# Performance work log

Measured on AMD Instinct MI355X. Metric: run time of the kernel, lower is better.

The kernel has to match this reference:

```python
import jax, jax.numpy as jnp
import numpy as np

B, LP, LQ, H = 32, 2048, 512, 1024

def setup_inputs() -> dict:
    key = jax.random.key(0)
    k1, k2, k3, k4 = jax.random.split(key, 4)
    p_encode = jax.random.normal(k1, (B, LP, H), dtype=jnp.float32)
    q_encode = jax.random.normal(k2, (B, LQ, H), dtype=jnp.float32)
    # nn.Linear(H, H): weight [out, in], bias [out]
    bound = 1.0 / np.sqrt(H)
    G_weight = jax.random.uniform(k3, (H, H), dtype=jnp.float32, minval=-bound, maxval=bound)
    G_bias = jax.random.uniform(k4, (H,), dtype=jnp.float32, minval=-bound, maxval=bound)
    return {"p_encode": p_encode, "q_encode": q_encode, "G_weight": G_weight, "G_bias": G_bias}

def reference(p_encode, q_encode, G_weight, G_bias):
    # q_project = transpose(G(q_encode), -2, -1): [B, H, LQ]
    q_proj = jnp.einsum('bqh,oh->bqo', q_encode, G_weight) + G_bias  # [B, LQ, H]
    # att_matrix = bmm(p_encode, q_project^T): [B, LP, LQ]
    att = jnp.einsum('bph,bqh->bpq', p_encode, q_proj)
    # m_p = softmax over LQ (dim=-1) @ q_encode -> [B, LP, H]
    m_p = jnp.einsum('bpq,bqh->bph', jax.nn.softmax(att, axis=-1), q_encode)
    # m_q = softmax over LP (dim=-2), transposed, @ p_encode -> [B, LQ, H]
    m_q = jnp.einsum('bpq,bph->bqh', jax.nn.softmax(att, axis=-2), p_encode)
    return (m_p, m_q)
```

## Files before the change

kernel.cpp:

```cpp
#include <hip/hip_runtime.h>

typedef _Float16 half_t;
typedef _Float16 f16x8 __attribute__((ext_vector_type(8)));
typedef _Float16 f16x4 __attribute__((ext_vector_type(4)));
typedef float    f32x4 __attribute__((ext_vector_type(4)));
typedef float    f32x16 __attribute__((ext_vector_type(16)));

typedef const __attribute__((address_space(1))) void cg_void;
typedef __attribute__((address_space(3))) void lds_void;

#define BB 32
#define LP 2048
#define LQ 512
#define HH 1024

enum { M_QPROJ = 0, M_OUT32 = 1 };

__global__ void cvt16_k(const float* __restrict__ w, half_t* __restrict__ o) {
  long i = ((long)blockIdx.x * 256 + threadIdx.x) * 4;
  f32x4 v = *(const f32x4*)(w + i);
  f16x4 h;
  h[0] = (half_t)v[0]; h[1] = (half_t)v[1]; h[2] = (half_t)v[2]; h[3] = (half_t)v[3];
  *(f16x4*)(o + i) = h;
}

__global__ __launch_bounds__(256) void dualcvt_k(const float* __restrict__ in,
                                                 half_t* __restrict__ rm,
                                                 half_t* __restrict__ tr,
                                                 int R, int C) {
  __shared__ half_t tile[64 * 64];
  const long zb = blockIdx.z;
  const float* src = in + zb * (long)R * C;
  half_t* dstT = tr + zb * (long)C * R;
  half_t* dstR = rm + zb * (long)R * C;
  const int r0 = blockIdx.y * 64, c0 = blockIdx.x * 64;
  const int t = threadIdx.x;
  const int cl = (t & 15) * 4;
  const int rl = t >> 4;
#pragma unroll
  for (int rr = 0; rr < 4; rr++) {
    int r = rr * 16 + rl;
    f32x4 v = *(const f32x4*)(src + (long)(r0 + r) * C + c0 + cl);
    f16x4 h;
#pragma unroll
    for (int j = 0; j < 4; j++) {
      h[j] = (half_t)v[j];
      int c = cl + j;
      tile[c * 64 + (r ^ (((c >> 3) & 7) << 3))] = h[j];
    }
    *(f16x4*)(dstR + (long)(r0 + r) * C + c0 + cl) = h;
  }
  __syncthreads();
  const int c = t >> 2;
  const int rch = (t & 3) * 16;
  const int m = (c >> 3) & 7;
  const int B0 = c * 64 + (rch ^ ((m << 3) & 48));
  const int hi = (m & 1) << 3;
  f16x8 g0 = *(const f16x8*)&tile[B0 + hi];
  f16x8 g1 = *(const f16x8*)&tile[B0 + (8 ^ hi)];
  half_t* dp = dstT + (long)(c0 + c) * R + r0 + rch;
  *(f16x8*)dp = g0;
  *(f16x8*)(dp + 8) = g1;
}

__global__ __launch_bounds__(256) void cfin_k(const float* __restrict__ pmg,
                                              const float* __restrict__ psg,
                                              float* __restrict__ cmax,
                                              float* __restrict__ cinv) {
  long i = (long)blockIdx.x * 256 + threadIdx.x;
  long b = i / LQ, q = i - b * LQ;
  const float* mp = pmg + (b * 16) * LQ + q;
  const float* sp = psg + (b * 16) * LQ + q;
  float m = -3e38f, s = 0.f;
#pragma unroll
  for (int t = 0; t < 16; t++) {
    float mm = mp[(long)t * LQ], ss = sp[(long)t * LQ];
    float nm = fmaxf(m, mm);
    s = s * __expf(m - nm) + ss * __expf(mm - nm);
    m = nm;
  }
  cmax[i] = m;
  cinv[i] = 1.f / s;
}

__global__ __launch_bounds__(256) void pq_k(const half_t* __restrict__ E,
                                            half_t* __restrict__ out,
                                            const float* __restrict__ pmg,
                                            const float* __restrict__ cmax,
                                            const float* __restrict__ cinv) {
  __shared__ half_t tile[64 * 64];
  const long zb = blockIdx.z;
  const half_t* src = E + zb * (long)LP * LQ;
  half_t* dst = out + zb * (long)LQ * LP;
  const int r0 = blockIdx.y * 64, c0 = blockIdx.x * 64;
  const int tIdx = r0 >> 7;
  const int t = threadIdx.x;
  const int cl = (t & 15) * 4;
  const int rl = t >> 4;
  f32x4 tm = *(const f32x4*)(pmg + ((long)zb * 16 + tIdx) * LQ + c0 + cl);
  f32x4 cm = *(const f32x4*)(cmax + (long)zb * LQ + c0 + cl);
  f32x4 ci = *(const f32x4*)(cinv + (long)zb * LQ + c0 + cl);
  float sc[4];
#pragma unroll
  for (int j = 0; j < 4; j++) sc[j] = __expf(tm[j] - cm[j]) * ci[j];
#pragma unroll
  for (int rr = 0; rr < 4; rr++) {
    int r = rr * 16 + rl;
    f16x4 v = *(const f16x4*)(src + (long)(r0 + r) * LQ + c0 + cl);
#pragma unroll
    for (int j = 0; j < 4; j++) {
      float x = (float)v[j] * sc[j];
      int c = cl + j;
      tile[c * 64 + (r ^ (((c >> 3) & 7) << 3))] = (half_t)x;
    }
  }
  __syncthreads();
  const int c = t >> 2;
  const int rch = (t & 3) * 16;
  const int m = (c >> 3) & 7;
  const int B0 = c * 64 + (rch ^ ((m << 3) & 48));
  const int hi = (m & 1) << 3;
  f16x8 g0 = *(const f16x8*)&tile[B0 + hi];
  f16x8 g1 = *(const f16x8*)&tile[B0 + (8 ^ hi)];
  half_t* dp = dst + (long)(c0 + c) * LP + r0 + rch;
  *(f16x8*)dp = g0;
  *(f16x8*)(dp + 8) = g1;
}

template<int ROWS>
__device__ __forceinline__ void stage_op(const half_t* src, int ld,
                                         half_t* lds_base, int wid, int lane) {
  const int goff = (((lane & 3) ^ ((lane >> 3) & 3)) << 3);
#pragma unroll
  for (int j = 0; j < ROWS / 128; ++j) {
    int row = j * 128 + wid * 16 + (lane >> 2);
    const half_t* g = src + (long)row * ld + goff;
    __builtin_amdgcn_global_load_lds((cg_void*)g,
        (lds_void*)(lds_base + j * 4096 + wid * 512), 16, 0, 0);
  }
}

__device__ __forceinline__ void xcd_swz(long lid, long nwg, long& out) {
  const long q8 = nwg >> 3, r8 = nwg & 7;
  const long xcd = lid & 7, rest = lid >> 3;
  out = (xcd < r8 ? xcd * (q8 + 1) : r8 * (q8 + 1) + (xcd - r8) * q8) + rest;
}

__global__ __launch_bounds__(512, 2) void attf_k(
    const half_t* __restrict__ Ap,
    const half_t* __restrict__ Bp,
    half_t* __restrict__ PpO,
    half_t* __restrict__ EO,
    float* __restrict__ pmg, float* __restrict__ psg) {
  __shared__ __align__(16) half_t As[3 * 4096];
  __shared__ __align__(16) half_t Bs[3 * 16384];
  __shared__ float rmL[4][128];
  __shared__ float cmL[2][512];
  __shared__ float rsL[4][128];
  __shared__ float csL[2][512];

  const int nby = gridDim.y;
  long lid;
  xcd_swz(blockIdx.y + (long)nby * blockIdx.z, (long)nby * gridDim.z, lid);
  const int by = (int)(lid % nby);
  const int bz = (int)(lid / nby);

  const int t0 = threadIdx.x;
  const int lane = t0 & 63;
  const int wid = t0 >> 6;
  const int wm = wid >> 2, wn = wid & 3;
  const int m0 = by * 128;

  const half_t* Abase = Ap + ((long)bz * LP + m0) * HH;
  const half_t* Bbase = Bp + (long)bz * LQ * HH;

  const int c5 = lane & 31, hi = lane >> 5;
  const int sx = (c5 >> 1) & 3;
  const int ofs0 = c5 * 32 + ((hi ^ sx) << 3);
  const int ofs1 = c5 * 32 + (((2 | hi) ^ sx) << 3);

  f32x16 acc[2][4] = {};
  const int NT = HH / 32;

#pragma unroll
  for (int tt = 0; tt < 2; ++tt) {
    stage_op<128>(Abase + tt * 32, HH, As + tt * 4096, wid, lane);
    stage_op<512>(Bbase + tt * 32, HH, Bs + tt * 16384, wid, lane);
  }

  for (int t = 0; t < NT; ++t) {
    if (t + 1 < NT) asm volatile("s_waitcnt vmcnt(5)" ::: "memory");
    else            asm volatile("s_waitcnt vmcnt(0)" ::: "memory");
    __builtin_amdgcn_s_barrier();
    asm volatile("" ::: "memory");

    const half_t* Au = As + (t % 3) * 4096;
    const half_t* Bu = Bs + (t % 3) * 16384;
    f16x8 af[2][2], bf[4][2];
#pragma unroll
    for (int mf = 0; mf < 2; ++mf) {
      const half_t* p = Au + (wm * 64 + mf * 32) * 32;
      af[mf][0] = *(const f16x8*)(p + ofs0);
      af[mf][1] = *(const f16x8*)(p + ofs1);
    }
#pragma unroll
    for (int nf = 0; nf < 4; ++nf) {
      const half_t* p = Bu + (wn * 128 + nf * 32) * 32;
      bf[nf][0] = *(const f16x8*)(p + ofs0);
      bf[nf][1] = *(const f16x8*)(p + ofs1);
    }
    if (t + 2 < NT) {
      const int u2 = (t + 2) % 3;
      stage_op<128>(Abase + (t + 2) * 32, HH, As + u2 * 4096, wid, lane);
      stage_op<512>(Bbase + (t + 2) * 32, HH, Bs + u2 * 16384, wid, lane);
    }
    __builtin_amdgcn_s_setprio(1);
#pragma unroll
    for (int mf = 0; mf < 2; ++mf)
#pragma unroll
      for (int nf = 0; nf < 4; ++nf) {
        acc[mf][nf] = __builtin_amdgcn_mfma_f32_32x32x16_f16(af[mf][0], bf[nf][0], acc[mf][nf], 0, 0, 0);
        acc[mf][nf] = __builtin_amdgcn_mfma_f32_32x32x16_f16(af[mf][1], bf[nf][1], acc[mf][nf], 0, 0, 0);
      }
    __builtin_amdgcn_s_setprio(0);
  }

  float rmv[2][16], cmv[4];
#pragma unroll
  for (int m = 0; m < 2; ++m)
#pragma unroll
    for (int r = 0; r < 16; ++r) {
      float v = fmaxf(fmaxf(acc[m][0][r], acc[m][1][r]), fmaxf(acc[m][2][r], acc[m][3][r]));
#pragma unroll
      for (int o = 1; o < 32; o <<= 1) v = fmaxf(v, __shfl_xor(v, o, 64));
      rmv[m][r] = v;
    }
#pragma unroll
  for (int n = 0; n < 4; ++n) {
    float v = acc[0][n][0];
#pragma unroll
    for (int m = 0; m < 2; ++m)
#pragma unroll
      for (int r = 0; r < 16; ++r) v = fmaxf(v, acc[m][n][r]);
    v = fmaxf(v, __shfl_xor(v, 32, 64));
    cmv[n] = v;
  }
  if (c5 < 16) {
#pragma unroll
    for (int m = 0; m < 2; ++m)
      rmL[wn][wm * 64 + m * 32 + (c5 & 3) + 8 * (c5 >> 2) + 4 * hi] = rmv[m][c5];
  }
  if (hi == 0) {
#pragma unroll
    for (int n = 0; n < 4; ++n) cmL[wm][wn * 128 + n * 32 + c5] = cmv[n];
  }
  __syncthreads();
  if (t0 < 128)
    rmL[0][t0] = fmaxf(fmaxf(rmL[0][t0], rmL[1][t0]), fmaxf(rmL[2][t0], rmL[3][t0]));
  {
    float cm2 = fmaxf(cmL[0][t0 & 511], cmL[1][t0 & 511]);
    cmL[0][t0 & 511] = cm2;
    pmg[((long)bz * 16 + by) * LQ + (t0 & 511)] = cm2;
  }
  __syncthreads();
#pragma unroll
  for (int m = 0; m < 2; ++m)
#pragma unroll
    for (int r = 0; r < 16; ++r)
      rmv[m][r] = rmL[0][wm * 64 + m * 32 + (r & 3) + 8 * (r >> 2) + 4 * hi];
#pragma unroll
  for (int n = 0; n < 4; ++n) cmv[n] = cmL[0][wn * 128 + n * 32 + c5];

  half_t* EB = EO + (long)bz * LP * LQ;
  float csW[4] = {0.f, 0.f, 0.f, 0.f};
  float rowS[2][16];
#pragma unroll
  for (int m = 0; m < 2; ++m)
#pragma unroll
    for (int r = 0; r < 16; ++r) {
      long grow = (long)(m0 + wm * 64 + m * 32 + (r & 3) + 8 * (r >> 2) + 4 * hi) * LQ;
      float s = 0.f;
#pragma unroll
      for (int n = 0; n < 4; ++n) {
        float a = acc[m][n][r];
        float e = __expf(a - cmv[n]);
        float p = __expf(a - rmv[m][r]);
        csW[n] += e;
        EB[grow + wn * 128 + n * 32 + c5] = (half_t)e;
        acc[m][n][r] = p;
        s += p;
      }
#pragma unroll
      for (int o = 1; o < 32; o <<= 1) s += __shfl_xor(s, o, 64);
      rowS[m][r] = s;
    }
#pragma unroll
  for (int n = 0; n < 4; ++n) csW[n] += __shfl_xor(csW[n], 32, 64);
  if (c5 < 16) {
#pragma unroll
    for (int m = 0; m < 2; ++m)
      rsL[wn][wm * 64 + m * 32 + (c5 & 3) + 8 * (c5 >> 2) + 4 * hi] = rowS[m][c5];
  }
  if (hi == 0) {
#pragma unroll
    for (int n = 0; n < 4; ++n) csL[wm][wn * 128 + n * 32 + c5] = csW[n];
  }
  __syncthreads();
  if (t0 < 128)
    rsL[0][t0] = 1.f / (rsL[0][t0] + rsL[1][t0] + rsL[2][t0] + rsL[3][t0]);
  psg[((long)bz * 16 + by) * LQ + (t0 & 511)] = csL[0][t0 & 511] + csL[1][t0 & 511];
  __syncthreads();

  half_t* PpB = PpO + (long)bz * LP * LQ;
#pragma unroll
  for (int m = 0; m < 2; ++m)
#pragma unroll
    for (int r = 0; r < 16; ++r) {
      int row = wm * 64 + m * 32 + (r & 3) + 8 * (r >> 2) + 4 * hi;
      long grow = (long)(m0 + row) * LQ;
      float ri = rsL[0][row];
#pragma unroll
      for (int n = 0; n < 4; ++n)
        PpB[grow + wn * 128 + n * 32 + c5] = (half_t)(acc[m][n][r] * ri);
    }
}

template<int MODE, int BM>
__global__ __launch_bounds__(512, 2) void gemm_k(
    const half_t* __restrict__ Ap, const half_t* __restrict__ Bp, void* __restrict__ Cp,
    const float* __restrict__ bias,
    int lda, int ldb, int ldc, int K,
    long sA, long sB, long sC) {
  constexpr int NMF = BM / 64;
  constexpr int AS = BM * 32;
  __shared__ __align__(16) half_t As[4 * AS];
  __shared__ __align__(16) half_t Bs[4 * 8192];

  const int nbx = gridDim.x, nby = gridDim.y;
  long lid;
  xcd_swz(blockIdx.x + (long)nbx * (blockIdx.y + (long)nby * blockIdx.z),
          (long)nbx * nby * gridDim.z, lid);
  const int bx = (int)(lid % nbx);
  const long tmp = lid / nbx;
  const int by = (int)(tmp % nby);
  const int bz = (int)(tmp / nby);

  const int t0 = threadIdx.x;
  const int lane = t0 & 63;
  const int wid = t0 >> 6;
  const int wm = wid >> 2, wn = wid & 3;
  const int m0 = by * BM, n0 = bx * 256;

  const half_t* Abase = Ap + sA * bz + (long)m0 * lda;
  const half_t* Bbase = Bp + sB * bz + (long)n0 * ldb;

  const int c5 = lane & 31, hi = lane >> 5;
  const int sx = (c5 >> 1) & 3;
  const int ofs0 = c5 * 32 + ((hi ^ sx) << 3);
  const int ofs1 = c5 * 32 + (((2 | hi) ^ sx) << 3);

  f32x16 acc[NMF][2] = {};
  const int NT = K >> 5;

#pragma unroll
  for (int tt = 0; tt < 3; ++tt) {
    stage_op<BM>(Abase + tt * 32, lda, As + tt * AS, wid, lane);
    stage_op<256>(Bbase + tt * 32, ldb, Bs + tt * 8192, wid, lane);
  }

  for (int t = 0; t < NT; ++t) {
    if (t + 2 < NT) {
      if constexpr (BM == 256) asm volatile("s_waitcnt vmcnt(8)" ::: "memory");
      else                     asm volatile("s_waitcnt vmcnt(6)" ::: "memory");
    } else if (t + 1 < NT) {
      if constexpr (BM == 256) asm volatile("s_waitcnt vmcnt(4)" ::: "memory");
      else                     asm volatile("s_waitcnt vmcnt(3)" ::: "memory");
    } else {
      asm volatile("s_waitcnt vmcnt(0)" ::: "memory");
    }
    __builtin_amdgcn_s_barrier();
    asm volatile("" ::: "memory");

    const half_t* Au = As + (t & 3) * AS;
    const half_t* Bu = Bs + (t & 3) * 8192;
    f16x8 af[NMF][2], bf[2][2];
#pragma unroll
    for (int mf = 0; mf < NMF; ++mf) {
      const half_t* p = Au + (wm * (BM / 2) + mf * 32) * 32;
      af[mf][0] = *(const f16x8*)(p + ofs0);
      af[mf][1] = *(const f16x8*)(p + ofs1);
    }
#pragma unroll
    for (int nf = 0; nf < 2; ++nf) {
      const half_t* p = Bu + (wn * 64 + nf * 32) * 32;
      bf[nf][0] = *(const f16x8*)(p + ofs0);
      bf[nf][1] = *(const f16x8*)(p + ofs1);
    }
    if (t + 3 < NT) {
      const int u3 = (t + 3) & 3;
      stage_op<BM>(Abase + (t + 3) * 32, lda, As + u3 * AS, wid, lane);
      stage_op<256>(Bbase + (t + 3) * 32, ldb, Bs + u3 * 8192, wid, lane);
    }
    __builtin_amdgcn_s_setprio(1);
#pragma unroll
    for (int mf = 0; mf < NMF; ++mf)
#pragma unroll
      for (int nf = 0; nf < 2; ++nf) {
        acc[mf][nf] = __builtin_amdgcn_mfma_f32_32x32x16_f16(af[mf][0], bf[nf][0], acc[mf][nf], 0, 0, 0);
        acc[mf][nf] = __builtin_amdgcn_mfma_f32_32x32x16_f16(af[mf][1], bf[nf][1], acc[mf][nf], 0, 0, 0);
      }
    __builtin_amdgcn_s_setprio(0);
  }

#pragma unroll
  for (int nf = 0; nf < 2; ++nf) {
    int col = n0 + wn * 64 + nf * 32 + c5;
    float bv = 0.f;
    if constexpr (MODE == M_QPROJ) bv = bias[col];
#pragma unroll
    for (int mf = 0; mf < NMF; ++mf) {
      int rbase = m0 + wm * (BM / 2) + mf * 32 + 4 * hi;
#pragma unroll
      for (int r = 0; r < 16; ++r) {
        int row = rbase + (r & 3) + 8 * (r >> 2);
        if constexpr (MODE == M_QPROJ)
          ((half_t*)Cp)[(long)row * ldc + col] = (half_t)(acc[mf][nf][r] + bv);
        else
          ((float*)Cp)[sC * bz + (long)row * ldc + col] = acc[mf][nf][r];
      }
    }
  }
}

extern "C" void kernel_launch(void* const* d_in, const int* in_sizes, int n_in,
                              void* d_out, int out_size, void* d_ws, size_t ws_size,
                              hipStream_t stream) {
  const float* p_enc = (const float*)d_in[0];
  const float* q_enc = (const float*)d_in[1];
  const float* Gw    = (const float*)d_in[2];
  const float* Gb    = (const float*)d_in[3];
  float* m_p = (float*)d_out;
  float* m_q = m_p + (long)BB * LP * HH;

  half_t* w16   = (half_t*)d_ws;
  half_t* q16   = w16 + (long)HH * HH;
  half_t* qT16  = q16 + (long)BB * LQ * HH;
  half_t* qpj16 = qT16 + (long)BB * HH * LQ;
  half_t* p16   = qpj16 + (long)BB * LQ * HH;
  half_t* pT16  = p16 + (long)BB * LP * HH;
  half_t* Pp    = pT16 + (long)BB * HH * LP;
  half_t* Ebuf  = Pp + (long)BB * LP * LQ;
  half_t* Pq    = Ebuf + (long)BB * LP * LQ;
  float*  cmaxb = (float*)(Pq + (long)BB * LQ * LP);
  float*  cinvb = cmaxb + (long)BB * LQ;
  float*  pmg   = cinvb + (long)BB * LQ;
  float*  psg   = pmg + (long)BB * 16 * LQ;

  cvt16_k<<<HH * HH / 1024, 256, 0, stream>>>(Gw, w16);

  dualcvt_k<<<dim3(HH / 64, LQ / 64, BB), 256, 0, stream>>>(q_enc, q16, qT16, LQ, HH);

  gemm_k<M_QPROJ, 256><<<dim3(HH / 256, BB * LQ / 256, 1), 512, 0, stream>>>(
      q16, w16, qpj16, Gb, HH, HH, HH, HH, 0, 0, 0);

  dualcvt_k<<<dim3(HH / 64, LP / 64, BB), 256, 0, stream>>>(p_enc, p16, pT16, LP, HH);

  attf_k<<<dim3(1, LP / 128, BB), 512, 0, stream>>>(p16, qpj16, Pp, Ebuf, pmg, psg);

  cfin_k<<<BB * LQ / 256, 256, 0, stream>>>(pmg, psg, cmaxb, cinvb);
  pq_k<<<dim3(LQ / 64, LP / 64, BB), 256, 0, stream>>>(Ebuf, Pq, pmg, cmaxb, cinvb);

  gemm_k<M_OUT32, 256><<<dim3(HH / 256, LP / 256, BB), 512, 0, stream>>>(
      Pp, qT16, m_p, nullptr, LQ, LQ, HH, LQ,
      (long)LP * LQ, (long)HH * LQ, (long)LP * HH);

  gemm_k<M_OUT32, 256><<<dim3(HH / 256, LQ / 256, BB), 512, 0, stream>>>(
      Pq, pT16, m_q, nullptr, LP, LP, HH, LP,
      (long)LQ * LP, (long)HH * LP, (long)LQ * HH);
}
```

Before: 535.4 us.

## Merge conversion, column-softmax finalize, and output GEMM launches into fewer kernels

```diff
diff --git a/kernel.cpp b/kernel.cpp
--- a/kernel.cpp
+++ b/kernel.cpp
@@ -24,16 +24,23 @@
   *(f16x4*)(o + i) = h;
 }
 
-__global__ __launch_bounds__(256) void dualcvt_k(const float* __restrict__ in,
-                                                 half_t* __restrict__ rm,
-                                                 half_t* __restrict__ tr,
-                                                 int R, int C) {
+__global__ __launch_bounds__(256) void cvt2_k(const float* __restrict__ qe,
+                                              half_t* __restrict__ q16o,
+                                              half_t* __restrict__ qT16o,
+                                              const float* __restrict__ pe,
+                                              half_t* __restrict__ p16o,
+                                              half_t* __restrict__ pT16o) {
   __shared__ half_t tile[64 * 64];
+  const int byg = blockIdx.y;
+  const float* in; half_t* rm; half_t* tr; int R, r0;
+  if (byg < 8) { in = qe; rm = q16o; tr = qT16o; R = LQ; r0 = byg * 64; }
+  else         { in = pe; rm = p16o; tr = pT16o; R = LP; r0 = (byg - 8) * 64; }
+  const int C = HH;
   const long zb = blockIdx.z;
   const float* src = in + zb * (long)R * C;
   half_t* dstT = tr + zb * (long)C * R;
   half_t* dstR = rm + zb * (long)R * C;
-  const int r0 = blockIdx.y * 64, c0 = blockIdx.x * 64;
+  const int c0 = blockIdx.x * 64;
   const int t = threadIdx.x;
   const int cl = (t & 15) * 4;
   const int rl = t >> 4;
@@ -63,31 +70,10 @@
   *(f16x8*)(dp + 8) = g1;
 }
 
-__global__ __launch_bounds__(256) void cfin_k(const float* __restrict__ pmg,
-                                              const float* __restrict__ psg,
-                                              float* __restrict__ cmax,
-                                              float* __restrict__ cinv) {
-  long i = (long)blockIdx.x * 256 + threadIdx.x;
-  long b = i / LQ, q = i - b * LQ;
-  const float* mp = pmg + (b * 16) * LQ + q;
-  const float* sp = psg + (b * 16) * LQ + q;
-  float m = -3e38f, s = 0.f;
-#pragma unroll
-  for (int t = 0; t < 16; t++) {
-    float mm = mp[(long)t * LQ], ss = sp[(long)t * LQ];
-    float nm = fmaxf(m, mm);
-    s = s * __expf(m - nm) + ss * __expf(mm - nm);
-    m = nm;
-  }
-  cmax[i] = m;
-  cinv[i] = 1.f / s;
-}
-
-__global__ __launch_bounds__(256) void pq_k(const half_t* __restrict__ E,
-                                            half_t* __restrict__ out,
-                                            const float* __restrict__ pmg,
-                                            const float* __restrict__ cmax,
-                                            const float* __restrict__ cinv) {
+__global__ __launch_bounds__(256) void pq2_k(const half_t* __restrict__ E,
+                                             half_t* __restrict__ out,
+                                             const float* __restrict__ pmg,
+                                             const float* __restrict__ psg) {
   __shared__ half_t tile[64 * 64];
   const long zb = blockIdx.z;
   const half_t* src = E + zb * (long)LP * LQ;
@@ -97,12 +83,26 @@
   const int t = threadIdx.x;
   const int cl = (t & 15) * 4;
   const int rl = t >> 4;
-  f32x4 tm = *(const f32x4*)(pmg + ((long)zb * 16 + tIdx) * LQ + c0 + cl);
-  f32x4 cm = *(const f32x4*)(cmax + (long)zb * LQ + c0 + cl);
-  f32x4 ci = *(const f32x4*)(cinv + (long)zb * LQ + c0 + cl);
+
+  float m4[4] = {-3e38f, -3e38f, -3e38f, -3e38f}, s4[4] = {0.f, 0.f, 0.f, 0.f};
+  const float* mpb = pmg + (long)zb * 16 * LQ + c0 + cl;
+  const float* spb = psg + (long)zb * 16 * LQ + c0 + cl;
+#pragma unroll
+  for (int tt = 0; tt < 16; ++tt) {
+    f32x4 mm = *(const f32x4*)(mpb + (long)tt * LQ);
+    f32x4 ss = *(const f32x4*)(spb + (long)tt * LQ);
+#pragma unroll
+    for (int j = 0; j < 4; ++j) {
+      float nm = fmaxf(m4[j], mm[j]);
+      s4[j] = s4[j] * __expf(m4[j] - nm) + ss[j] * __expf(mm[j] - nm);
+      m4[j] = nm;
+    }
+  }
+  f32x4 tm = *(const f32x4*)(mpb + (long)tIdx * LQ);
   float sc[4];
 #pragma unroll
-  for (int j = 0; j < 4; j++) sc[j] = __expf(tm[j] - cm[j]) * ci[j];
+  for (int j = 0; j < 4; ++j) sc[j] = __expf(tm[j] - m4[j]) / s4[j];
+
 #pragma unroll
   for (int rr = 0; rr < 4; rr++) {
     int r = rr * 16 + rl;
@@ -325,34 +325,20 @@
     }
 }
 
-template<int MODE, int BM>
-__global__ __launch_bounds__(512, 2) void gemm_k(
-    const half_t* __restrict__ Ap, const half_t* __restrict__ Bp, void* __restrict__ Cp,
-    const float* __restrict__ bias,
-    int lda, int ldb, int ldc, int K,
-    long sA, long sB, long sC) {
-  constexpr int NMF = BM / 64;
-  constexpr int AS = BM * 32;
-  __shared__ __align__(16) half_t As[4 * AS];
+template<int MODE>
+__device__ __forceinline__ void gemm_core(const half_t* __restrict__ Abase,
+                                          const half_t* __restrict__ Bbase,
+                                          void* __restrict__ cB,
+                                          const float* __restrict__ biasB,
+                                          int lda, int ldb, int ldc, int K) {
+  constexpr int NMF = 4;
+  __shared__ __align__(16) half_t As[4 * 8192];
   __shared__ __align__(16) half_t Bs[4 * 8192];
-
-  const int nbx = gridDim.x, nby = gridDim.y;
-  long lid;
-  xcd_swz(blockIdx.x + (long)nbx * (blockIdx.y + (long)nby * blockIdx.z),
-          (long)nbx * nby * gridDim.z, lid);
-  const int bx = (int)(lid % nbx);
-  const long tmp = lid / nbx;
-  const int by = (int)(tmp % nby);
-  const int bz = (int)(tmp / nby);
 
   const int t0 = threadIdx.x;
   const int lane = t0 & 63;
   const int wid = t0 >> 6;
   const int wm = wid >> 2, wn = wid & 3;
-  const int m0 = by * BM, n0 = bx * 256;
-
-  const half_t* Abase = Ap + sA * bz + (long)m0 * lda;
-  const half_t* Bbase = Bp + sB * bz + (long)n0 * ldb;
 
   const int c5 = lane & 31, hi = lane >> 5;
   const int sx = (c5 >> 1) & 3;
@@ -364,29 +350,23 @@
 
 #pragma unroll
   for (int tt = 0; tt < 3; ++tt) {
-    stage_op<BM>(Abase + tt * 32, lda, As + tt * AS, wid, lane);
+    stage_op<256>(Abase + tt * 32, lda, As + tt * 8192, wid, lane);
     stage_op<256>(Bbase + tt * 32, ldb, Bs + tt * 8192, wid, lane);
   }
 
   for (int t = 0; t < NT; ++t) {
-    if (t + 2 < NT) {
-      if constexpr (BM == 256) asm volatile("s_waitcnt vmcnt(8)" ::: "memory");
-      else                     asm volatile("s_waitcnt vmcnt(6)" ::: "memory");
-    } else if (t + 1 < NT) {
-      if constexpr (BM == 256) asm volatile("s_waitcnt vmcnt(4)" ::: "memory");
-      else                     asm volatile("s_waitcnt vmcnt(3)" ::: "memory");
-    } else {
-      asm volatile("s_waitcnt vmcnt(0)" ::: "memory");
-    }
+    if (t + 2 < NT)      asm volatile("s_waitcnt vmcnt(8)" ::: "memory");
+    else if (t + 1 < NT) asm volatile("s_waitcnt vmcnt(4)" ::: "memory");
+    else                 asm volatile("s_waitcnt vmcnt(0)" ::: "memory");
     __builtin_amdgcn_s_barrier();
     asm volatile("" ::: "memory");
 
-    const half_t* Au = As + (t & 3) * AS;
+    const half_t* Au = As + (t & 3) * 8192;
     const half_t* Bu = Bs + (t & 3) * 8192;
     f16x8 af[NMF][2], bf[2][2];
 #pragma unroll
     for (int mf = 0; mf < NMF; ++mf) {
-      const half_t* p = Au + (wm * (BM / 2) + mf * 32) * 32;
+      const half_t* p = Au + (wm * 128 + mf * 32) * 32;
       af[mf][0] = *(const f16x8*)(p + ofs0);
       af[mf][1] = *(const f16x8*)(p + ofs1);
     }
@@ -398,7 +378,7 @@
     }
     if (t + 3 < NT) {
       const int u3 = (t + 3) & 3;
-      stage_op<BM>(Abase + (t + 3) * 32, lda, As + u3 * AS, wid, lane);
+      stage_op<256>(Abase + (t + 3) * 32, lda, As + u3 * 8192, wid, lane);
       stage_op<256>(Bbase + (t + 3) * 32, ldb, Bs + u3 * 8192, wid, lane);
     }
     __builtin_amdgcn_s_setprio(1);
@@ -414,21 +394,60 @@
 
 #pragma unroll
   for (int nf = 0; nf < 2; ++nf) {
-    int col = n0 + wn * 64 + nf * 32 + c5;
+    int col = wn * 64 + nf * 32 + c5;
     float bv = 0.f;
-    if constexpr (MODE == M_QPROJ) bv = bias[col];
+    if constexpr (MODE == M_QPROJ) bv = biasB[col];
 #pragma unroll
     for (int mf = 0; mf < NMF; ++mf) {
-      int rbase = m0 + wm * (BM / 2) + mf * 32 + 4 * hi;
+      int rbase = wm * 128 + mf * 32 + 4 * hi;
 #pragma unroll
       for (int r = 0; r < 16; ++r) {
         int row = rbase + (r & 3) + 8 * (r >> 2);
         if constexpr (MODE == M_QPROJ)
-          ((half_t*)Cp)[(long)row * ldc + col] = (half_t)(acc[mf][nf][r] + bv);
+          ((half_t*)cB)[(long)row * ldc + col] = (half_t)(acc[mf][nf][r] + bv);
         else
-          ((float*)Cp)[sC * bz + (long)row * ldc + col] = acc[mf][nf][r];
+          ((float*)cB)[(long)row * ldc + col] = acc[mf][nf][r];
       }
     }
+  }
+}
+
+__global__ __launch_bounds__(512, 2) void gemmq_k(const half_t* __restrict__ q16,
+                                                  const half_t* __restrict__ w16,
+                                                  half_t* __restrict__ qpj,
+                                                  const float* __restrict__ Gb) {
+  const int nbx = gridDim.x, nby = gridDim.y;
+  long lid;
+  xcd_swz(blockIdx.x + (long)nbx * blockIdx.y, (long)nbx * nby, lid);
+  const int bx = (int)(lid % nbx);
+  const int by = (int)(lid / nbx);
+  gemm_core<M_QPROJ>(q16 + (long)(by * 256) * HH,
+                     w16 + (long)(bx * 256) * HH,
+                     qpj + (long)(by * 256) * HH + bx * 256,
+                     Gb + bx * 256, HH, HH, HH, HH);
+}
+
+__global__ __launch_bounds__(512, 2) void gemm2_k(
+    const half_t* __restrict__ Pp, const half_t* __restrict__ qT16, float* __restrict__ m_p,
+    const half_t* __restrict__ Pq, const half_t* __restrict__ pT16, float* __restrict__ m_q) {
+  long lid;
+  xcd_swz(blockIdx.x + 4L * (blockIdx.y + 10L * blockIdx.z), 4L * 10 * 32, lid);
+  const int bx = (int)(lid % 4);
+  const long tmp = lid / 4;
+  const int by = (int)(tmp % 10);
+  const int bz = (int)(tmp / 10);
+
+  if (by < 8) {
+    gemm_core<M_OUT32>(Pp + (long)bz * LP * LQ + (long)(by * 256) * LQ,
+                       qT16 + (long)bz * HH * LQ + (long)(bx * 256) * LQ,
+                       m_p + (long)bz * LP * HH + (long)(by * 256) * HH + bx * 256,
+                       nullptr, LQ, LQ, HH, LQ);
+  } else {
+    const int qy = by - 8;
+    gemm_core<M_OUT32>(Pq + (long)bz * LQ * LP + (long)(qy * 256) * LP,
+                       pT16 + (long)bz * HH * LP + (long)(bx * 256) * LP,
+                       m_q + (long)bz * LQ * HH + (long)(qy * 256) * HH + bx * 256,
+                       nullptr, LP, LP, HH, LP);
   }
 }
 
@@ -451,30 +470,18 @@
   half_t* Pp    = pT16 + (long)BB * HH * LP;
   half_t* Ebuf  = Pp + (long)BB * LP * LQ;
   half_t* Pq    = Ebuf + (long)BB * LP * LQ;
-  float*  cmaxb = (float*)(Pq + (long)BB * LQ * LP);
-  float*  cinvb = cmaxb + (long)BB * LQ;
-  float*  pmg   = cinvb + (long)BB * LQ;
+  float*  pmg   = (float*)(Pq + (long)BB * LQ * LP);
   float*  psg   = pmg + (long)BB * 16 * LQ;
 
   cvt16_k<<<HH * HH / 1024, 256, 0, stream>>>(Gw, w16);
 
-  dualcvt_k<<<dim3(HH / 64, LQ / 64, BB), 256, 0, stream>>>(q_enc, q16, qT16, LQ, HH);
-
-  gemm_k<M_QPROJ, 256><<<dim3(HH / 256, BB * LQ / 256, 1), 512, 0, stream>>>(
-      q16, w16, qpj16, Gb, HH, HH, HH, HH, 0, 0, 0);
-
-  dualcvt_k<<<dim3(HH / 64, LP / 64, BB), 256, 0, stream>>>(p_enc, p16, pT16, LP, HH);
+  cvt2_k<<<dim3(HH / 64, 40, BB), 256, 0, stream>>>(q_enc, q16, qT16, p_enc, p16, pT16);
+
+  gemmq_k<<<dim3(HH / 256, BB * LQ / 256, 1), 512, 0, stream>>>(q16, w16, qpj16, Gb);
 
   attf_k<<<dim3(1, LP / 128, BB), 512, 0, stream>>>(p16, qpj16, Pp, Ebuf, pmg, psg);
 
-  cfin_k<<<BB * LQ / 256, 256, 0, stream>>>(pmg, psg, cmaxb, cinvb);
-  pq_k<<<dim3(LQ / 64, LP / 64, BB), 256, 0, stream>>>(Ebuf, Pq, pmg, cmaxb, cinvb);
-
-  gemm_k<M_OUT32, 256><<<dim3(HH / 256, LP / 256, BB), 512, 0, stream>>>(
-      Pp, qT16, m_p, nullptr, LQ, LQ, HH, LQ,
-      (long)LP * LQ, (long)HH * LQ, (long)LP * HH);
-
-  gemm_k<M_OUT32, 256><<<dim3(HH / 256, LQ / 256, BB), 512, 0, stream>>>(
-      Pq, pT16, m_q, nullptr, LP, LP, HH, LP,
-      (long)LQ * LP, (long)HH * LP, (long)LQ * HH);
-}
+  pq2_k<<<dim3(LQ / 64, LP / 64, BB), 256, 0, stream>>>(Ebuf, Pq, pmg, psg);
+
+  gemm2_k<<<dim3(4, 10, BB), 512, 0, stream>>>(Pp, qT16, m_p, Pq, pT16, m_q);
+}
```

Measured after the change: 566.2 us. 5.7% more time.

## Replace 256x256 GEMM with 128x128 double-buffered tile and merge launches

Applied to the files above, without the earlier changes.

```diff
diff --git a/kernel.cpp b/kernel.cpp
--- a/kernel.cpp
+++ b/kernel.cpp
@@ -24,16 +24,23 @@
   *(f16x4*)(o + i) = h;
 }
 
-__global__ __launch_bounds__(256) void dualcvt_k(const float* __restrict__ in,
-                                                 half_t* __restrict__ rm,
-                                                 half_t* __restrict__ tr,
-                                                 int R, int C) {
+__global__ __launch_bounds__(256) void cvt2_k(const float* __restrict__ qe,
+                                              half_t* __restrict__ q16o,
+                                              half_t* __restrict__ qT16o,
+                                              const float* __restrict__ pe,
+                                              half_t* __restrict__ p16o,
+                                              half_t* __restrict__ pT16o) {
   __shared__ half_t tile[64 * 64];
+  const int byg = blockIdx.y;
+  const float* in; half_t* rm; half_t* tr; int R, r0;
+  if (byg < 8) { in = qe; rm = q16o; tr = qT16o; R = LQ; r0 = byg * 64; }
+  else         { in = pe; rm = p16o; tr = pT16o; R = LP; r0 = (byg - 8) * 64; }
+  const int C = HH;
   const long zb = blockIdx.z;
   const float* src = in + zb * (long)R * C;
   half_t* dstT = tr + zb * (long)C * R;
   half_t* dstR = rm + zb * (long)R * C;
-  const int r0 = blockIdx.y * 64, c0 = blockIdx.x * 64;
+  const int c0 = blockIdx.x * 64;
   const int t = threadIdx.x;
   const int cl = (t & 15) * 4;
   const int rl = t >> 4;
@@ -140,6 +147,18 @@
   }
 }
 
+__device__ __forceinline__ void stage4(const half_t* src, int ld,
+                                       half_t* lds_base, int wid, int lane) {
+  const int goff = (((lane & 3) ^ ((lane >> 3) & 3)) << 3);
+#pragma unroll
+  for (int j = 0; j < 2; ++j) {
+    int row = j * 64 + wid * 16 + (lane >> 2);
+    const half_t* g = src + (long)row * ld + goff;
+    __builtin_amdgcn_global_load_lds((cg_void*)g,
+        (lds_void*)(lds_base + j * 2048 + wid * 512), 16, 0, 0);
+  }
+}
+
 __device__ __forceinline__ void xcd_swz(long lid, long nwg, long& out) {
   const long q8 = nwg >> 3, r8 = nwg & 7;
   const long xcd = lid & 7, rest = lid >> 3;
@@ -147,10 +166,8 @@
 }
 
 __global__ __launch_bounds__(512, 2) void attf_k(
-    const half_t* __restrict__ Ap,
-    const half_t* __restrict__ Bp,
-    half_t* __restrict__ PpO,
-    half_t* __restrict__ EO,
+    const half_t* __restrict__ Ap, const half_t* __restrict__ Bp,
+    half_t* __restrict__ PpO, half_t* __restrict__ EO,
     float* __restrict__ pmg, float* __restrict__ psg) {
   __shared__ __align__(16) half_t As[3 * 4096];
   __shared__ __align__(16) half_t Bs[3 * 16384];
@@ -325,110 +342,107 @@
     }
 }
 
-template<int MODE, int BM>
-__global__ __launch_bounds__(512, 2) void gemm_k(
-    const half_t* __restrict__ Ap, const half_t* __restrict__ Bp, void* __restrict__ Cp,
-    const float* __restrict__ bias,
-    int lda, int ldb, int ldc, int K,
-    long sA, long sB, long sC) {
-  constexpr int NMF = BM / 64;
-  constexpr int AS = BM * 32;
-  __shared__ __align__(16) half_t As[4 * AS];
-  __shared__ __align__(16) half_t Bs[4 * 8192];
-
-  const int nbx = gridDim.x, nby = gridDim.y;
-  long lid;
-  xcd_swz(blockIdx.x + (long)nbx * (blockIdx.y + (long)nby * blockIdx.z),
-          (long)nbx * nby * gridDim.z, lid);
-  const int bx = (int)(lid % nbx);
-  const long tmp = lid / nbx;
-  const int by = (int)(tmp % nby);
-  const int bz = (int)(tmp / nby);
+template<int MODE>
+__device__ __forceinline__ void core97(const half_t* __restrict__ Ab,
+                                       const half_t* __restrict__ Bb,
+                                       void* __restrict__ cB,
+                                       const float* __restrict__ biasB,
+                                       int lda, int ldb, int ldc, int K) {
+  __shared__ __align__(16) half_t As[2][4096];
+  __shared__ __align__(16) half_t Bs[2][4096];
 
   const int t0 = threadIdx.x;
   const int lane = t0 & 63;
   const int wid = t0 >> 6;
-  const int wm = wid >> 2, wn = wid & 3;
-  const int m0 = by * BM, n0 = bx * 256;
-
-  const half_t* Abase = Ap + sA * bz + (long)m0 * lda;
-  const half_t* Bbase = Bp + sB * bz + (long)n0 * ldb;
-
-  const int c5 = lane & 31, hi = lane >> 5;
-  const int sx = (c5 >> 1) & 3;
-  const int ofs0 = c5 * 32 + ((hi ^ sx) << 3);
-  const int ofs1 = c5 * 32 + (((2 | hi) ^ sx) << 3);
-
-  f32x16 acc[NMF][2] = {};
+  const int wm = wid >> 1, wn = wid & 1;
+  const int fr = lane & 15, fs = lane >> 4;
+  const int fbase = fr * 32 + ((fs ^ ((fr >> 1) & 3)) << 3);
+
+  f32x4 acc[4][4] = {};
   const int NT = K >> 5;
 
-#pragma unroll
-  for (int tt = 0; tt < 3; ++tt) {
-    stage_op<BM>(Abase + tt * 32, lda, As + tt * AS, wid, lane);
-    stage_op<256>(Bbase + tt * 32, ldb, Bs + tt * 8192, wid, lane);
-  }
-
+  stage4(Ab, lda, As[0], wid, lane);
+  stage4(Bb, ldb, Bs[0], wid, lane);
+  __syncthreads();
+
+  int cur = 0;
   for (int t = 0; t < NT; ++t) {
-    if (t + 2 < NT) {
-      if constexpr (BM == 256) asm volatile("s_waitcnt vmcnt(8)" ::: "memory");
-      else                     asm volatile("s_waitcnt vmcnt(6)" ::: "memory");
-    } else if (t + 1 < NT) {
-      if constexpr (BM == 256) asm volatile("s_waitcnt vmcnt(4)" ::: "memory");
-      else                     asm volatile("s_waitcnt vmcnt(3)" ::: "memory");
-    } else {
-      asm volatile("s_waitcnt vmcnt(0)" ::: "memory");
-    }
-    __builtin_amdgcn_s_barrier();
-    asm volatile("" ::: "memory");
-
-    const half_t* Au = As + (t & 3) * AS;
-    const half_t* Bu = Bs + (t & 3) * 8192;
-    f16x8 af[NMF][2], bf[2][2];
-#pragma unroll
-    for (int mf = 0; mf < NMF; ++mf) {
-      const half_t* p = Au + (wm * (BM / 2) + mf * 32) * 32;
-      af[mf][0] = *(const f16x8*)(p + ofs0);
-      af[mf][1] = *(const f16x8*)(p + ofs1);
-    }
-#pragma unroll
-    for (int nf = 0; nf < 2; ++nf) {
-      const half_t* p = Bu + (wn * 64 + nf * 32) * 32;
-      bf[nf][0] = *(const f16x8*)(p + ofs0);
-      bf[nf][1] = *(const f16x8*)(p + ofs1);
-    }
-    if (t + 3 < NT) {
-      const int u3 = (t + 3) & 3;
-      stage_op<BM>(Abase + (t + 3) * 32, lda, As + u3 * AS, wid, lane);
-      stage_op<256>(Bbase + (t + 3) * 32, ldb, Bs + u3 * 8192, wid, lane);
-    }
+    if (t + 1 < NT) {
+      stage4(Ab + (t + 1) * 32, lda, As[cur ^ 1], wid, lane);
+      stage4(Bb + (t + 1) * 32, ldb, Bs[cur ^ 1], wid, lane);
+    }
+    f16x8 af[4], bf[4];
+#pragma unroll
+    for (int f = 0; f < 4; ++f) af[f] = *(const f16x8*)&As[cur][(wm * 64 + f * 16) * 32 + fbase];
+#pragma unroll
+    for (int f = 0; f < 4; ++f) bf[f] = *(const f16x8*)&Bs[cur][(wn * 64 + f * 16) * 32 + fbase];
     __builtin_amdgcn_s_setprio(1);
 #pragma unroll
-    for (int mf = 0; mf < NMF; ++mf)
-#pragma unroll
-      for (int nf = 0; nf < 2; ++nf) {
-        acc[mf][nf] = __builtin_amdgcn_mfma_f32_32x32x16_f16(af[mf][0], bf[nf][0], acc[mf][nf], 0, 0, 0);
-        acc[mf][nf] = __builtin_amdgcn_mfma_f32_32x32x16_f16(af[mf][1], bf[nf][1], acc[mf][nf], 0, 0, 0);
+    for (int fm = 0; fm < 4; ++fm)
+#pragma unroll
+      for (int fn = 0; fn < 4; ++fn)
+        acc[fm][fn] = __builtin_amdgcn_mfma_f32_16x16x32_f16(af[fm], bf[fn], acc[fm][fn], 0, 0, 0);
+    __builtin_amdgcn_s_setprio(0);
+    __syncthreads();
+    cur ^= 1;
+  }
+
+  const int r0 = (lane >> 4) * 4;
+#pragma unroll
+  for (int fn = 0; fn < 4; ++fn) {
+    int col = wn * 64 + fn * 16 + fr;
+    float bv = 0.f;
+    if constexpr (MODE == M_QPROJ) bv = biasB[col];
+#pragma unroll
+    for (int fm = 0; fm < 4; ++fm) {
+      int row = wm * 64 + fm * 16 + r0;
+#pragma unroll
+      for (int j = 0; j < 4; j++) {
+        if constexpr (MODE == M_QPROJ)
+          ((half_t*)cB)[(long)(row + j) * ldc + col] = (half_t)(acc[fm][fn][j] + bv);
+        else
+          ((float*)cB)[(long)(row + j) * ldc + col] = acc[fm][fn][j];
       }
-    __builtin_amdgcn_s_setprio(0);
-  }
-
-#pragma unroll
-  for (int nf = 0; nf < 2; ++nf) {
-    int col = n0 + wn * 64 + nf * 32 + c5;
-    float bv = 0.f;
-    if constexpr (MODE == M_QPROJ) bv = bias[col];
-#pragma unroll
-    for (int mf = 0; mf < NMF; ++mf) {
-      int rbase = m0 + wm * (BM / 2) + mf * 32 + 4 * hi;
-#pragma unroll
-      for (int r = 0; r < 16; ++r) {
-        int row = rbase + (r & 3) + 8 * (r >> 2);
-        if constexpr (MODE == M_QPROJ)
-          ((half_t*)Cp)[(long)row * ldc + col] = (half_t)(acc[mf][nf][r] + bv);
-        else
-          ((float*)Cp)[sC * bz + (long)row * ldc + col] = acc[mf][nf][r];
-      }
-    }
+    }
+  }
+}
+
+__global__ __launch_bounds__(256, 3) void gemmq_k(const half_t* __restrict__ q16,
+                                                  const half_t* __restrict__ w16,
+                                                  half_t* __restrict__ qpj,
+                                                  const float* __restrict__ Gb) {
+  const int nbx = gridDim.x, nby = gridDim.y;
+  long lid;
+  xcd_swz(blockIdx.x + (long)nbx * blockIdx.y, (long)nbx * nby, lid);
+  const int bx = (int)(lid % nbx);
+  const int by = (int)(lid / nbx);
+  core97<M_QPROJ>(q16 + (long)(by * 128) * HH,
+                  w16 + (long)(bx * 128) * HH,
+                  qpj + (long)(by * 128) * HH + bx * 128,
+                  Gb + bx * 128, HH, HH, HH, HH);
+}
+
+__global__ __launch_bounds__(256, 3) void gemm2_k(
+    const half_t* __restrict__ Pp, const half_t* __restrict__ qT16, float* __restrict__ m_p,
+    const half_t* __restrict__ Pq, const half_t* __restrict__ pT16, float* __restrict__ m_q) {
+  long lid;
+  xcd_swz(blockIdx.x + 8L * (blockIdx.y + 20L * blockIdx.z), 8L * 20 * 32, lid);
+  const int bx = (int)(lid % 8);
+  const long tmp = lid / 8;
+  const int by = (int)(tmp % 20);
+  const int bz = (int)(tmp / 20);
+
+  if (by < 16) {
+    core97<M_OUT32>(Pp + (long)bz * LP * LQ + (long)(by * 128) * LQ,
+                    qT16 + (long)bz * HH * LQ + (long)(bx * 128) * LQ,
+                    m_p + (long)bz * LP * HH + (long)(by * 128) * HH + bx * 128,
+                    nullptr, LQ, LQ, HH, LQ);
+  } else {
+    const int qy = by - 16;
+    core97<M_OUT32>(Pq + (long)bz * LQ * LP + (long)(qy * 128) * LP,
+                    pT16 + (long)bz * HH * LP + (long)(bx * 128) * LP,
+                    m_q + (long)bz * LQ * HH + (long)(qy * 128) * HH + bx * 128,
+                    nullptr, LP, LP, HH, LP);
   }
 }
 
@@ -458,23 +472,14 @@
 
   cvt16_k<<<HH * HH / 1024, 256, 0, stream>>>(Gw, w16);
 
-  dualcvt_k<<<dim3(HH / 64, LQ / 64, BB), 256, 0, stream>>>(q_enc, q16, qT16, LQ, HH);
-
-  gemm_k<M_QPROJ, 256><<<dim3(HH / 256, BB * LQ / 256, 1), 512, 0, stream>>>(
-      q16, w16, qpj16, Gb, HH, HH, HH, HH, 0, 0, 0);
-
-  dualcvt_k<<<dim3(HH / 64, LP / 64, BB), 256, 0, stream>>>(p_enc, p16, pT16, LP, HH);
+  cvt2_k<<<dim3(HH / 64, 40, BB), 256, 0, stream>>>(q_enc, q16, qT16, p_enc, p16, pT16);
+
+  gemmq_k<<<dim3(HH / 128, BB * LQ / 128, 1), 256, 0, stream>>>(q16, w16, qpj16, Gb);
 
   attf_k<<<dim3(1, LP / 128, BB), 512, 0, stream>>>(p16, qpj16, Pp, Ebuf, pmg, psg);
 
   cfin_k<<<BB * LQ / 256, 256, 0, stream>>>(pmg, psg, cmaxb, cinvb);
   pq_k<<<dim3(LQ / 64, LP / 64, BB), 256, 0, stream>>>(Ebuf, Pq, pmg, cmaxb, cinvb);
 
-  gemm_k<M_OUT32, 256><<<dim3(HH / 256, LP / 256, BB), 512, 0, stream>>>(
-      Pp, qT16, m_p, nullptr, LQ, LQ, HH, LQ,
-      (long)LP * LQ, (long)HH * LQ, (long)LP * HH);
-
-  gemm_k<M_OUT32, 256><<<dim3(HH / 256, LQ / 256, BB), 512, 0, stream>>>(
-      Pq, pT16, m_q, nullptr, LP, LP, HH, LP,
-      (long)LQ * LP, (long)HH * LP, (long)LQ * HH);
-}
+  gemm2_k<<<dim3(8, 20, BB), 256, 0, stream>>>(Pp, qT16, m_p, Pq, pT16, m_q);
+}
```

Result: slower. 552.3 us (+3.2%).
